# Kernel optimization log

Measured on AMD Instinct MI355X. Metric: run time of the kernel, lower is better.

The kernel has to match this reference:

```python
import jax, jax.numpy as jnp
import numpy as np

BATCH_SIZE = 512
N_PARTS = 4
TEMP_FAC = 0.1
D = 4096
EPS = 1e-6


def _static_indices():
    # bs and factor per the n_parts==4, batch_size!=12 branch
    bs = 4 * BATCH_SIZE
    factor = 10 * N_PARTS
    pos = np.arange(bs)
    active = pos[pos % (3 * N_PARTS) < N_PARTS]            # positions that contribute
    # i1..i6 = (pos + k*n_parts) % bs for k = 0..5
    I = (active[:, None] + np.arange(6)[None, :] * N_PARTS) % bs   # (P, 6)
    # denominator indices removed: (pos + k*n_parts) % bs for k = 0..factor*n_parts-1
    offs = (active[:, None] + np.arange(factor * N_PARTS)[None, :] * N_PARTS) % bs
    M = np.ones((active.shape[0], bs), dtype=np.float32)
    M[np.arange(active.shape[0])[:, None], offs] = 0.0     # (P, bs) denominator mask
    return I, M

_I, _M = _static_indices()
# symmetrical-loss pairs: (i1,i2),(i2,i3),(i1,i4),(i4,i5),(i5,i6),(i2,i5),(i3,i6)
_PAIRS = [(0, 1), (1, 2), (0, 3), (3, 4), (4, 5), (1, 4), (2, 5)]


def setup_inputs() -> dict:
    key = jax.random.key(0)
    reg_pred = jax.random.normal(key, (4 * BATCH_SIZE, D), dtype=jnp.float32)
    return {"reg_pred": reg_pred}


def reference(reg_pred):
    I = jnp.asarray(_I)
    M = jnp.asarray(_M)
    norms = jnp.linalg.norm(reg_pred, axis=1)              # (bs,)
    # torch CosineSimilarity: dot / max(||a||*||b||, eps)
    gram = reg_pred @ reg_pred.T                           # (bs, bs)
    S = gram / jnp.maximum(norms[:, None] * norms[None, :], EPS) / TEMP_FAC
    E = jnp.exp(S)                                         # (bs, bs)
    # denominator exp-sums for each anchor role k at each active position p
    Dsum = jnp.einsum('pkb,pb->pk', E[I], M)               # (P, 6)
    total = jnp.float32(0.0)
    for a, b in _PAIRS:
        num = S[I[:, a], I[:, b]]                          # (P,)
        en = jnp.exp(num)
        total = total + jnp.sum(-jnp.log(en / (en + Dsum[:, a]))
                                - jnp.log(en / (en + Dsum[:, b])))
    return total / (6 * BATCH_SIZE)
```

## Files before the change

### kernel.cpp

```cpp
#include <hip/hip_runtime.h>
#include <hip/hip_bf16.h>
#include <stdint.h>

#define NROWS 2048
#define DIM   4096
#define NACT  684
#define INV_TEMP 10.0f
#define NTILE 136
#define KSPLIT 4
#define KSEG  1024
#define KITER 32
#define FP8_SCALE 16.0f
#define PART_SCALE (1.0f / 256.0f)

#define WAITCNT_VM0   0x0F70
#define WAITCNT_VM2   0x0F72
#define WAITCNT_VM4   0x0F74
#define WAITCNT_VM6   0x0F76

typedef __attribute__((ext_vector_type(4))) float floatx4;
typedef __attribute__((ext_vector_type(8))) short shortx8;
typedef __attribute__((ext_vector_type(8))) unsigned short ushortx8;

static __device__ __forceinline__ unsigned short f32_to_bf16(float f) {
  union { float f; unsigned int u; } v; v.f = f;
  unsigned int u = v.u;
  unsigned int r = u + 0x7fffu + ((u >> 16) & 1u);
  return (unsigned short)(r >> 16);
}
static __device__ __forceinline__ float bf16_to_f32(unsigned short u) {
  union { unsigned int u; float f; } v; v.u = ((unsigned int)u) << 16;
  return v.f;
}
static __device__ __forceinline__ unsigned short f32_to_f16(float f) {
  _Float16 h = (_Float16)f;
  union { _Float16 h; unsigned short u; } v; v.h = h;
  return v.u;
}
static __device__ __forceinline__ float f16_to_f32(unsigned short u) {
  union { unsigned short u; _Float16 h; } v; v.u = u;
  return (float)v.h;
}

__global__ __launch_bounds__(256) void k_normconv_fp8(const float* __restrict__ X,
                                                      unsigned char* __restrict__ Yq) {
  const int row = blockIdx.x;
  const float4* xr = (const float4*)(X + (size_t)row * DIM);
  float4 v[4];
  float s = 0.f;
#pragma unroll
  for (int t = 0; t < 4; t++) {
    float4 w = xr[threadIdx.x * 4 + t];
    v[t] = w;
    s += w.x * w.x + w.y * w.y + w.z * w.z + w.w * w.w;
  }
#pragma unroll
  for (int off = 32; off > 0; off >>= 1) s += __shfl_down(s, off, 64);
  __shared__ float wsum[4];
  if ((threadIdx.x & 63) == 0) wsum[threadIdx.x >> 6] = s;
  __syncthreads();
  const float total = wsum[0] + wsum[1] + wsum[2] + wsum[3];
  const float sc = FP8_SCALE / fmaxf(sqrtf(total), 1e-30f);
  uint4 o;
  unsigned int r0;
  r0 = __builtin_amdgcn_cvt_pk_fp8_f32(v[0].x * sc, v[0].y * sc, 0, false);
  o.x = __builtin_amdgcn_cvt_pk_fp8_f32(v[0].z * sc, v[0].w * sc, r0, true);
  r0 = __builtin_amdgcn_cvt_pk_fp8_f32(v[1].x * sc, v[1].y * sc, 0, false);
  o.y = __builtin_amdgcn_cvt_pk_fp8_f32(v[1].z * sc, v[1].w * sc, r0, true);
  r0 = __builtin_amdgcn_cvt_pk_fp8_f32(v[2].x * sc, v[2].y * sc, 0, false);
  o.z = __builtin_amdgcn_cvt_pk_fp8_f32(v[2].z * sc, v[2].w * sc, r0, true);
  r0 = __builtin_amdgcn_cvt_pk_fp8_f32(v[3].x * sc, v[3].y * sc, 0, false);
  o.w = __builtin_amdgcn_cvt_pk_fp8_f32(v[3].z * sc, v[3].w * sc, r0, true);
  ((uint4*)(Yq + (size_t)row * DIM))[threadIdx.x] = o;
}

__global__ __launch_bounds__(256) void k_gemm_sym(const unsigned char* __restrict__ Yq,
                                                  unsigned short* __restrict__ P) {
  __shared__ __attribute__((aligned(16))) unsigned char lds[4 * 8192];
  const int bid = blockIdx.x;
  const int kz = bid & 3;
  const int t  = bid >> 2;
  int ti = 0, rem = t;
  while (rem >= 16 - ti) { rem -= 16 - ti; ti++; }
  const int tj = ti + rem;
  const int row0 = ti * 128;
  const int col0 = tj * 128;
  const int kbase = kz * KSEG;

  const int tid  = threadIdx.x;
  const int lane = tid & 63;
  const int wave = tid >> 6;
  const int wr = wave >> 1;
  const int wc = wave & 1;

  floatx4 zero = {0.f, 0.f, 0.f, 0.f};
  floatx4 acc[4][4];
#pragma unroll
  for (int i = 0; i < 4; i++)
#pragma unroll
    for (int j = 0; j < 4; j++) acc[i][j] = zero;

  const unsigned char* gA = Yq + (size_t)(row0 + (tid >> 1)) * DIM + kbase + (tid & 1) * 16;
  const unsigned char* gB = Yq + (size_t)(col0 + (tid >> 1)) * DIM + kbase + (tid & 1) * 16;

  const int fr  = lane & 15;
  const int fc8 = (lane >> 4) * 8;

#define ISSUE(st, koff)                                                                \
  do {                                                                                 \
    __builtin_amdgcn_global_load_lds(                                                  \
        (const __attribute__((address_space(1))) void*)(gA + (koff)),                  \
        (__attribute__((address_space(3))) void*)(lds + (st) * 8192 + tid * 16),       \
        16, 0, 0);                                                                     \
    __builtin_amdgcn_global_load_lds(                                                  \
        (const __attribute__((address_space(1))) void*)(gB + (koff)),                  \
        (__attribute__((address_space(3))) void*)(lds + (st) * 8192 + 4096 + tid * 16),\
        16, 0, 0);                                                                     \
  } while (0)

#define COMPUTE(st)                                                                    \
  do {                                                                                 \
    const unsigned char* bA = lds + (st) * 8192;                                       \
    const unsigned char* bB = bA + 4096;                                               \
    long long af[4], bf[4];                                                            \
    _Pragma("unroll")                                                                  \
    for (int mi = 0; mi < 4; mi++)                                                     \
      af[mi] = *(const long long*)(bA + (wr * 64 + mi * 16 + fr) * 32 + fc8);          \
    _Pragma("unroll")                                                                  \
    for (int ni = 0; ni < 4; ni++)                                                     \
      bf[ni] = *(const long long*)(bB + (wc * 64 + ni * 16 + fr) * 32 + fc8);          \
    _Pragma("unroll")                                                                  \
    for (int mi = 0; mi < 4; mi++)                                                     \
      _Pragma("unroll")                                                                \
      for (int ni = 0; ni < 4; ni++)                                                   \
        acc[mi][ni] = __builtin_amdgcn_mfma_f32_16x16x32_fp8_fp8(af[mi], bf[ni],       \
                                                                 acc[mi][ni], 0, 0, 0);\
  } while (0)

  ISSUE(0, 0);
  ISSUE(1, 32);
  ISSUE(2, 64);
#pragma unroll 4
  for (int k = 0; k < KITER; k++) {
    const int cur = k & 3;
    if (k < KITER - 3) {
      ISSUE((k + 3) & 3, (k + 3) * 32);
      __builtin_amdgcn_s_waitcnt(WAITCNT_VM6);
    } else if (k == KITER - 3) {
      __builtin_amdgcn_s_waitcnt(WAITCNT_VM4);
    } else if (k == KITER - 2) {
      __builtin_amdgcn_s_waitcnt(WAITCNT_VM2);
    } else {
      __builtin_amdgcn_s_waitcnt(WAITCNT_VM0);
    }
    __builtin_amdgcn_sched_barrier(0);
    __builtin_amdgcn_s_barrier();
    COMPUTE(cur);
    if (k < KITER - 1) {
      __builtin_amdgcn_s_barrier();
      __builtin_amdgcn_sched_barrier(0);
    }
  }

#undef ISSUE
#undef COMPUTE

  unsigned short* dst = P + (size_t)(t * KSPLIT + kz) * 16384;
  const int cc  = lane & 15;
  const int cr4 = (lane >> 4) * 4;
#pragma unroll
  for (int mi = 0; mi < 4; mi++) {
    const int row = wr * 64 + mi * 16 + cr4;
#pragma unroll
    for (int ni = 0; ni < 4; ni++) {
      const int col = wc * 64 + ni * 16 + cc;
      unsigned int d0 = (unsigned int)f32_to_bf16(acc[mi][ni][0] * PART_SCALE) |
                        ((unsigned int)f32_to_bf16(acc[mi][ni][1] * PART_SCALE) << 16);
      unsigned int d1 = (unsigned int)f32_to_bf16(acc[mi][ni][2] * PART_SCALE) |
                        ((unsigned int)f32_to_bf16(acc[mi][ni][3] * PART_SCALE) << 16);
      uint2 v; v.x = d0; v.y = d1;
      *(uint2*)(dst + (size_t)col * 128 + row) = v;
    }
  }
}

__global__ __launch_bounds__(256) void k_combine(const unsigned short* __restrict__ P,
                                                 unsigned short* __restrict__ S,
                                                 float* __restrict__ T) {
  __shared__ float tileS[32][132];
  __shared__ float tileE[32][132];
  const int t = blockIdx.x;
  const int h = blockIdx.y;
  int ti = 0, rem = t;
  while (rem >= 16 - ti) { rem -= 16 - ti; ti++; }
  const int tj = ti + rem;
  const int gr = ti * 128, gc = tj * 128;
  const int c0 = h * 32;
  const int tid = threadIdx.x;
  const int cl = tid >> 3;
  const int q  = tid & 7;

  float acc[16];
#pragma unroll
  for (int j = 0; j < 16; j++) acc[j] = 0.f;
#pragma unroll
  for (int kz = 0; kz < KSPLIT; kz++) {
    const ushortx8* p = (const ushortx8*)(P + (size_t)(t * KSPLIT + kz) * 16384 +
                                          (size_t)(c0 + cl) * 128 + q * 16);
#pragma unroll
    for (int c = 0; c < 2; c++) {
      ushortx8 u = p[c];
#pragma unroll
      for (int e = 0; e < 8; e++) acc[c * 8 + e] += bf16_to_f32((unsigned short)u[e]);
    }
  }
  float cs = 0.f;
  unsigned short hv[16];
#pragma unroll
  for (int j = 0; j < 16; j++) {
    float v = acc[j] * INV_TEMP;
    float ev = __expf(v);
    hv[j] = f32_to_f16(v);
    tileS[cl][q * 16 + j] = v;
    tileE[cl][q * 16 + j] = ev;
    cs += ev;
  }
  {
    uint4* srow = (uint4*)(S + (size_t)(gc + c0 + cl) * NROWS + gr + q * 16);
#pragma unroll
    for (int u = 0; u < 2; u++) {
      uint4 w;
      w.x = (unsigned int)hv[u * 8 + 0] | ((unsigned int)hv[u * 8 + 1] << 16);
      w.y = (unsigned int)hv[u * 8 + 2] | ((unsigned int)hv[u * 8 + 3] << 16);
      w.z = (unsigned int)hv[u * 8 + 4] | ((unsigned int)hv[u * 8 + 5] << 16);
      w.w = (unsigned int)hv[u * 8 + 6] | ((unsigned int)hv[u * 8 + 7] << 16);
      srow[u] = w;
    }
  }
  cs += __shfl_xor(cs, 1, 64);
  cs += __shfl_xor(cs, 2, 64);
  cs += __shfl_xor(cs, 4, 64);
  if (q == 0) atomicAdd(&T[gc + c0 + cl], cs);

  if (ti != tj) {
    __syncthreads();
    const int r = tid >> 1;
    const int hh = tid & 1;
    float rs = 0.f;
    unsigned short hv2[16];
#pragma unroll
    for (int e = 0; e < 16; e++) {
      hv2[e] = f32_to_f16(tileS[hh * 16 + e][r]);
      rs += tileE[hh * 16 + e][r];
    }
    uint4* drow = (uint4*)(S + (size_t)(gr + r) * NROWS + gc + c0 + hh * 16);
#pragma unroll
    for (int u = 0; u < 2; u++) {
      uint4 w;
      w.x = (unsigned int)hv2[u * 8 + 0] | ((unsigned int)hv2[u * 8 + 1] << 16);
      w.y = (unsigned int)hv2[u * 8 + 2] | ((unsigned int)hv2[u * 8 + 3] << 16);
      w.z = (unsigned int)hv2[u * 8 + 4] | ((unsigned int)hv2[u * 8 + 5] << 16);
      w.w = (unsigned int)hv2[u * 8 + 6] | ((unsigned int)hv2[u * 8 + 7] << 16);
      drow[u] = w;
    }
    rs += __shfl_xor(rs, 1, 64);
    if (hh == 0) atomicAdd(&T[gr + r], rs);
  }
}

__global__ __launch_bounds__(64) void k_dsum_h(const unsigned short* __restrict__ S,
                                               const float* __restrict__ T,
                                               float* __restrict__ Ds) {
  const int p = blockIdx.x;
  const int k = blockIdx.y;
  const int a = 12 * (p >> 2) + (p & 3);
  const int lane = threadIdx.x;
  const int row = (a + 4 * k) & (NROWS - 1);
  const int m = a >> 2;
  const int c = a & 3;
  const uint2* sr = (const uint2*)(S + (size_t)row * NROWS);
  float s = 0.f;
  {
    uint2 v0 = sr[(m + lane) & 511];
    uint2 v1 = sr[(m + 64 + lane) & 511];
    unsigned short e0 = (c < 2) ? (unsigned short)(v0.x >> (16 * c))
                                : (unsigned short)(v0.y >> (16 * (c - 2)));
    unsigned short e1 = (c < 2) ? (unsigned short)(v1.x >> (16 * c))
                                : (unsigned short)(v1.y >> (16 * (c - 2)));
    s += __expf(f16_to_f32(e0)) + __expf(f16_to_f32(e1));
    if (lane < 32) {
      uint2 v2 = sr[(m + 128 + lane) & 511];
      unsigned short e2 = (c < 2) ? (unsigned short)(v2.x >> (16 * c))
                                  : (unsigned short)(v2.y >> (16 * (c - 2)));
      s += __expf(f16_to_f32(e2));
    }
  }
#pragma unroll
  for (int off = 32; off > 0; off >>= 1) s += __shfl_down(s, off, 64);
  if (lane == 0) Ds[p * 6 + k] = T[row] - s;
}

__global__ __launch_bounds__(256) void k_final_h(const unsigned short* __restrict__ S,
                                                 const float* __restrict__ Ds,
                                                 float* __restrict__ out) {
  const int pa[7] = {0, 1, 0, 3, 4, 1, 2};
  const int pb[7] = {1, 2, 3, 4, 5, 4, 5};
  const int idx = blockIdx.x * 256 + threadIdx.x;
  float s = 0.f;
  if (idx < NACT * 7) {
    const int p = idx / 7;
    const int q = idx - p * 7;
    const int a0 = 12 * (p >> 2) + (p & 3);
    const int ra = (a0 + 4 * pa[q]) & (NROWS - 1);
    const int rb = (a0 + 4 * pb[q]) & (NROWS - 1);
    const float num = f16_to_f32(S[(size_t)ra * NROWS + rb]);
    const float en = __expf(num);
    s = __logf(en + Ds[p * 6 + pa[q]]) + __logf(en + Ds[p * 6 + pb[q]]) - 2.f * num;
  }
#pragma unroll
  for (int off = 32; off > 0; off >>= 1) s += __shfl_down(s, off, 64);
  if ((threadIdx.x & 63) == 0) atomicAdd(out, s * (1.0f / (6.0f * 512.0f)));
}

__global__ __launch_bounds__(256) void k_normconv(const float* __restrict__ X,
                                                  unsigned short* __restrict__ Y) {
  const int row = blockIdx.x;
  const float4* xr = (const float4*)(X + (size_t)row * DIM);
  float4 v[4];
  float s = 0.f;
#pragma unroll
  for (int t = 0; t < 4; t++) {
    float4 w = xr[threadIdx.x + t * 256];
    v[t] = w;
    s += w.x * w.x + w.y * w.y + w.z * w.z + w.w * w.w;
  }
#pragma unroll
  for (int off = 32; off > 0; off >>= 1) s += __shfl_down(s, off, 64);
  __shared__ float wsum[4];
  if ((threadIdx.x & 63) == 0) wsum[threadIdx.x >> 6] = s;
  __syncthreads();
  const float total = wsum[0] + wsum[1] + wsum[2] + wsum[3];
  const float inv = 1.0f / fmaxf(sqrtf(total), 1e-30f);
  ushort4* yr = (ushort4*)(Y + (size_t)row * DIM);
#pragma unroll
  for (int t = 0; t < 4; t++) {
    float4 w = v[t];
    ushort4 o;
    o.x = f32_to_bf16(w.x * inv);
    o.y = f32_to_bf16(w.y * inv);
    o.z = f32_to_bf16(w.z * inv);
    o.w = f32_to_bf16(w.w * inv);
    yr[threadIdx.x + t * 256] = o;
  }
}

__global__ __launch_bounds__(256) void k_gemm(const unsigned short* __restrict__ Y,
                                              float* __restrict__ S) {
  __shared__ __attribute__((aligned(16))) unsigned short sA[128 * 32];
  __shared__ __attribute__((aligned(16))) unsigned short sB[128 * 32];
  const int tid  = threadIdx.x;
  const int lane = tid & 63;
  const int wave = tid >> 6;
  const int wr = wave >> 1;
  const int wc = wave & 1;
  const int row0 = blockIdx.y * 128;
  const int col0 = blockIdx.x * 128;

  floatx4 zero = {0.f, 0.f, 0.f, 0.f};
  floatx4 acc[4][4];
#pragma unroll
  for (int i = 0; i < 4; i++)
#pragma unroll
    for (int j = 0; j < 4; j++) acc[i][j] = zero;

  const int sr = tid >> 2;
  const int sc = (tid & 3) * 8;
  const unsigned short* gA0 = Y + (size_t)(row0 + sr) * DIM + sc;
  const unsigned short* gA1 = gA0 + (size_t)64 * DIM;
  const unsigned short* gB0 = Y + (size_t)(col0 + sr) * DIM + sc;
  const unsigned short* gB1 = gB0 + (size_t)64 * DIM;

  const int fr = lane & 15;
  const int fc = (lane >> 4) * 8;

  for (int k0 = 0; k0 < DIM; k0 += 32) {
    __builtin_amdgcn_global_load_lds(
        (const __attribute__((address_space(1))) void*)(gA0 + k0),
        (__attribute__((address_space(3))) void*)(sA + tid * 8), 16, 0, 0);
    __builtin_amdgcn_global_load_lds(
        (const __attribute__((address_space(1))) void*)(gA1 + k0),
        (__attribute__((address_space(3))) void*)(sA + 2048 + tid * 8), 16, 0, 0);
    __builtin_amdgcn_global_load_lds(
        (const __attribute__((address_space(1))) void*)(gB0 + k0),
        (__attribute__((address_space(3))) void*)(sB + tid * 8), 16, 0, 0);
    __builtin_amdgcn_global_load_lds(
        (const __attribute__((address_space(1))) void*)(gB1 + k0),
        (__attribute__((address_space(3))) void*)(sB + 2048 + tid * 8), 16, 0, 0);
    __syncthreads();

    shortx8 af[4], bf[4];
#pragma unroll
    for (int mi = 0; mi < 4; mi++)
      af[mi] = *(const shortx8*)(sA + (wr * 64 + mi * 16 + fr) * 32 + fc);
#pragma unroll
    for (int ni = 0; ni < 4; ni++)
      bf[ni] = *(const shortx8*)(sB + (wc * 64 + ni * 16 + fr) * 32 + fc);
#pragma unroll
    for (int mi = 0; mi < 4; mi++)
#pragma unroll
      for (int ni = 0; ni < 4; ni++)
        acc[mi][ni] = __builtin_amdgcn_mfma_f32_16x16x32_bf16(af[mi], bf[ni], acc[mi][ni], 0, 0, 0);
    __syncthreads();
  }

  const int cc  = lane & 15;
  const int cr4 = (lane >> 4) * 4;
#pragma unroll
  for (int mi = 0; mi < 4; mi++) {
    const int row = row0 + wr * 64 + mi * 16 + cr4;
#pragma unroll
    for (int ni = 0; ni < 4; ni++) {
      const int col = col0 + wc * 64 + ni * 16 + cc;
      float* dst = S + (size_t)row * NROWS + col;
#pragma unroll
      for (int r = 0; r < 4; r++) dst[(size_t)r * NROWS] = acc[mi][ni][r] * INV_TEMP;
    }
  }
}

__global__ __launch_bounds__(256) void k_rowsum(const float* __restrict__ S,
                                                float* __restrict__ T) {
  const int row = blockIdx.x;
  const float* sr = S + (size_t)row * NROWS;
  float s = 0.f;
  for (int b = threadIdx.x; b < NROWS; b += 256) s += __expf(sr[b]);
#pragma unroll
  for (int off = 32; off > 0; off >>= 1) s += __shfl_down(s, off, 64);
  __shared__ float wsum[4];
  if ((threadIdx.x & 63) == 0) wsum[threadIdx.x >> 6] = s;
  __syncthreads();
  if (threadIdx.x == 0) T[row] = wsum[0] + wsum[1] + wsum[2] + wsum[3];
}

__global__ __launch_bounds__(64) void k_dsum(const float* __restrict__ S,
                                             const float* __restrict__ T,
                                             float* __restrict__ Ds) {
  const int p = blockIdx.x;
  const int k = blockIdx.y;
  const int a = 12 * (p >> 2) + (p & 3);
  const int lane = threadIdx.x;
  const int row = (a + 4 * k) & (NROWS - 1);
  const int m = a >> 2;
  const int c = a & 3;
  const float4* sr4 = (const float4*)(S + (size_t)row * NROWS);
  float s = 0.f;
  {
    float4 v0 = sr4[(m + lane) & 511];
    float4 v1 = sr4[(m + 64 + lane) & 511];
    float e0 = c == 0 ? v0.x : c == 1 ? v0.y : c == 2 ? v0.z : v0.w;
    float e1 = c == 0 ? v1.x : c == 1 ? v1.y : c == 2 ? v1.z : v1.w;
    s += __expf(e0) + __expf(e1);
    if (lane < 32) {
      float4 v2 = sr4[(m + 128 + lane) & 511];
      float e2 = c == 0 ? v2.x : c == 1 ? v2.y : c == 2 ? v2.z : v2.w;
      s += __expf(e2);
    }
  }
#pragma unroll
  for (int off = 32; off > 0; off >>= 1) s += __shfl_down(s, off, 64);
  if (lane == 0) Ds[p * 6 + k] = T[row] - s;
}

__global__ __launch_bounds__(256) void k_final(const float* __restrict__ S,
                                               const float* __restrict__ Ds,
                                               float* __restrict__ out) {
  const int pa[7] = {0, 1, 0, 3, 4, 1, 2};
  const int pb[7] = {1, 2, 3, 4, 5, 4, 5};
  const int idx = blockIdx.x * 256 + threadIdx.x;
  float s = 0.f;
  if (idx < NACT * 7) {
    const int p = idx / 7;
    const int q = idx - p * 7;
    const int a0 = 12 * (p >> 2) + (p & 3);
    const int ra = (a0 + 4 * pa[q]) & (NROWS - 1);
    const int rb = (a0 + 4 * pb[q]) & (NROWS - 1);
    const float num = S[(size_t)ra * NROWS + rb];
    const float en = __expf(num);
    s = __logf(en + Ds[p * 6 + pa[q]]) + __logf(en + Ds[p * 6 + pb[q]]) - 2.f * num;
  }
#pragma unroll
  for (int off = 32; off > 0; off >>= 1) s += __shfl_down(s, off, 64);
  if ((threadIdx.x & 63) == 0) atomicAdd(out, s * (1.0f / (6.0f * 512.0f)));
}

extern "C" void kernel_launch(void* const* d_in, const int* in_sizes, int n_in,
                              void* d_out, int out_size, void* d_ws, size_t ws_size,
                              hipStream_t stream) {
  const float* X = (const float*)d_in[0];
  char* ws = (char*)d_ws;
  float* out = (float*)d_out;

  const size_t pOff = (size_t)32 * 1024 * 1024;
  const size_t pBytes = (size_t)NTILE * KSPLIT * 16384 * 2;
  const size_t needA = pOff + pBytes + 8192 + NACT * 6 * 4 + 256;

  hipMemsetAsync(out, 0, sizeof(float), stream);

  if (ws_size >= needA) {
    unsigned char* Yq = (unsigned char*)ws;
    unsigned short* S16 = (unsigned short*)(ws + (size_t)16 * 1024 * 1024);
    unsigned short* P = (unsigned short*)(ws + pOff);
    float* T  = (float*)(ws + pOff + pBytes);
    float* Ds = (float*)(ws + pOff + pBytes + 8192);
    hipMemsetAsync(T, 0, NROWS * sizeof(float), stream);
    hipLaunchKernelGGL(k_normconv_fp8, dim3(NROWS), dim3(256), 0, stream, X, Yq);
    hipLaunchKernelGGL(k_gemm_sym, dim3(NTILE * KSPLIT), dim3(256), 0, stream, Yq, P);
    hipLaunchKernelGGL(k_combine, dim3(NTILE, 4), dim3(256), 0, stream, P, S16, T);
    hipLaunchKernelGGL(k_dsum_h, dim3(NACT, 6), dim3(64), 0, stream, S16, T, Ds);
    hipLaunchKernelGGL(k_final_h, dim3((NACT * 7 + 255) / 256), dim3(256), 0, stream, S16, Ds, out);
  } else {
    unsigned short* Y = (unsigned short*)ws;
    float* S = (float*)(ws + (size_t)16 * 1024 * 1024);
    float* T  = (float*)(ws + pOff);
    float* Ds = (float*)(ws + pOff + 8192);
    hipLaunchKernelGGL(k_normconv, dim3(NROWS), dim3(256), 0, stream, X, Y);
    hipLaunchKernelGGL(k_gemm, dim3(16, 16), dim3(256), 0, stream, Y, S);
    hipLaunchKernelGGL(k_rowsum, dim3(NROWS), dim3(256), 0, stream, S, T);
    hipLaunchKernelGGL(k_dsum, dim3(NACT, 6), dim3(64), 0, stream, S, T, Ds);
    hipLaunchKernelGGL(k_final, dim3((NACT * 7 + 255) / 256), dim3(256), 0, stream, S, Ds, out);
  }
}
```

Baseline: 121.4 us.

## Use 256x256 symmetric GEMM tiles with 8-way K split and fuse tail kernels

```diff
diff --git a/kernel.cpp b/kernel.cpp
--- a/kernel.cpp
+++ b/kernel.cpp
@@ -6,17 +6,16 @@
 #define DIM   4096
 #define NACT  684
 #define INV_TEMP 10.0f
-#define NTILE 136
-#define KSPLIT 4
-#define KSEG  1024
-#define KITER 32
+#define NT256 36
+#define KSPLIT 8
+#define KSEG  512
+#define KITER 16
 #define FP8_SCALE 16.0f
 #define PART_SCALE (1.0f / 256.0f)
 
 #define WAITCNT_VM0   0x0F70
 #define WAITCNT_VM2   0x0F72
 #define WAITCNT_VM4   0x0F74
-#define WAITCNT_VM6   0x0F76
 
 typedef __attribute__((ext_vector_type(4))) float floatx4;
 typedef __attribute__((ext_vector_type(8))) short shortx8;
@@ -74,17 +73,17 @@
   ((uint4*)(Yq + (size_t)row * DIM))[threadIdx.x] = o;
 }
 
-__global__ __launch_bounds__(256) void k_gemm_sym(const unsigned char* __restrict__ Yq,
-                                                  unsigned short* __restrict__ P) {
-  __shared__ __attribute__((aligned(16))) unsigned char lds[4 * 8192];
+__global__ __launch_bounds__(512, 2) void k_gemm_sym(const unsigned char* __restrict__ Yq,
+                                                     unsigned short* __restrict__ P) {
+  __shared__ __attribute__((aligned(16))) unsigned char lds[3 * 16384];
   const int bid = blockIdx.x;
-  const int kz = bid & 3;
-  const int t  = bid >> 2;
+  const int kz = bid & 7;
+  const int t  = bid >> 3;
   int ti = 0, rem = t;
-  while (rem >= 16 - ti) { rem -= 16 - ti; ti++; }
+  while (rem >= 8 - ti) { rem -= 8 - ti; ti++; }
   const int tj = ti + rem;
-  const int row0 = ti * 128;
-  const int col0 = tj * 128;
+  const int row0 = ti * 256;
+  const int col0 = tj * 256;
   const int kbase = kz * KSEG;
 
   const int tid  = threadIdx.x;
@@ -94,11 +93,11 @@
   const int wc = wave & 1;
 
   floatx4 zero = {0.f, 0.f, 0.f, 0.f};
-  floatx4 acc[4][4];
+  floatx4 acc[4][8];
 #pragma unroll
   for (int i = 0; i < 4; i++)
 #pragma unroll
-    for (int j = 0; j < 4; j++) acc[i][j] = zero;
+    for (int j = 0; j < 8; j++) acc[i][j] = zero;
 
   const unsigned char* gA = Yq + (size_t)(row0 + (tid >> 1)) * DIM + kbase + (tid & 1) * 16;
   const unsigned char* gB = Yq + (size_t)(col0 + (tid >> 1)) * DIM + kbase + (tid & 1) * 16;
@@ -106,47 +105,44 @@
   const int fr  = lane & 15;
   const int fc8 = (lane >> 4) * 8;
 
-#define ISSUE(st, koff)                                                                \
-  do {                                                                                 \
-    __builtin_amdgcn_global_load_lds(                                                  \
-        (const __attribute__((address_space(1))) void*)(gA + (koff)),                  \
-        (__attribute__((address_space(3))) void*)(lds + (st) * 8192 + tid * 16),       \
-        16, 0, 0);                                                                     \
-    __builtin_amdgcn_global_load_lds(                                                  \
-        (const __attribute__((address_space(1))) void*)(gB + (koff)),                  \
-        (__attribute__((address_space(3))) void*)(lds + (st) * 8192 + 4096 + tid * 16),\
-        16, 0, 0);                                                                     \
+#define ISSUE(st, koff)                                                                 \
+  do {                                                                                  \
+    __builtin_amdgcn_global_load_lds(                                                   \
+        (const __attribute__((address_space(1))) void*)(gA + (koff)),                   \
+        (__attribute__((address_space(3))) void*)(lds + (st) * 16384 + tid * 16),       \
+        16, 0, 0);                                                                      \
+    __builtin_amdgcn_global_load_lds(                                                   \
+        (const __attribute__((address_space(1))) void*)(gB + (koff)),                   \
+        (__attribute__((address_space(3))) void*)(lds + (st) * 16384 + 8192 + tid * 16),\
+        16, 0, 0);                                                                      \
   } while (0)
 
-#define COMPUTE(st)                                                                    \
-  do {                                                                                 \
-    const unsigned char* bA = lds + (st) * 8192;                                       \
-    const unsigned char* bB = bA + 4096;                                               \
-    long long af[4], bf[4];                                                            \
-    _Pragma("unroll")                                                                  \
-    for (int mi = 0; mi < 4; mi++)                                                     \
-      af[mi] = *(const long long*)(bA + (wr * 64 + mi * 16 + fr) * 32 + fc8);          \
-    _Pragma("unroll")                                                                  \
-    for (int ni = 0; ni < 4; ni++)                                                     \
-      bf[ni] = *(const long long*)(bB + (wc * 64 + ni * 16 + fr) * 32 + fc8);          \
-    _Pragma("unroll")                                                                  \
-    for (int mi = 0; mi < 4; mi++)                                                     \
-      _Pragma("unroll")                                                                \
-      for (int ni = 0; ni < 4; ni++)                                                   \
-        acc[mi][ni] = __builtin_amdgcn_mfma_f32_16x16x32_fp8_fp8(af[mi], bf[ni],       \
-                                                                 acc[mi][ni], 0, 0, 0);\
+#define COMPUTE(st)                                                                     \
+  do {                                                                                  \
+    const unsigned char* bA = lds + (st) * 16384;                                       \
+    const unsigned char* bB = bA + 8192;                                                \
+    long long af[4], bf[8];                                                             \
+    _Pragma("unroll")                                                                   \
+    for (int mi = 0; mi < 4; mi++)                                                      \
+      af[mi] = *(const long long*)(bA + (wr * 64 + mi * 16 + fr) * 32 + fc8);           \
+    _Pragma("unroll")                                                                   \
+    for (int ni = 0; ni < 8; ni++)                                                      \
+      bf[ni] = *(const long long*)(bB + (wc * 128 + ni * 16 + fr) * 32 + fc8);          \
+    _Pragma("unroll")                                                                   \
+    for (int mi = 0; mi < 4; mi++)                                                      \
+      _Pragma("unroll")                                                                 \
+      for (int ni = 0; ni < 8; ni++)                                                    \
+        acc[mi][ni] = __builtin_amdgcn_mfma_f32_16x16x32_fp8_fp8(af[mi], bf[ni],        \
+                                                                 acc[mi][ni], 0, 0, 0); \
   } while (0)
 
   ISSUE(0, 0);
   ISSUE(1, 32);
-  ISSUE(2, 64);
-#pragma unroll 4
+#pragma unroll
   for (int k = 0; k < KITER; k++) {
-    const int cur = k & 3;
-    if (k < KITER - 3) {
-      ISSUE((k + 3) & 3, (k + 3) * 32);
-      __builtin_amdgcn_s_waitcnt(WAITCNT_VM6);
-    } else if (k == KITER - 3) {
+    const int cur = k % 3;
+    if (k < KITER - 2) {
+      ISSUE((k + 2) % 3, (k + 2) * 32);
       __builtin_amdgcn_s_waitcnt(WAITCNT_VM4);
     } else if (k == KITER - 2) {
       __builtin_amdgcn_s_waitcnt(WAITCNT_VM2);
@@ -165,21 +161,21 @@
 #undef ISSUE
 #undef COMPUTE
 
-  unsigned short* dst = P + (size_t)(t * KSPLIT + kz) * 16384;
+  unsigned short* dst = P + (size_t)(t * KSPLIT + kz) * 65536;
   const int cc  = lane & 15;
   const int cr4 = (lane >> 4) * 4;
 #pragma unroll
   for (int mi = 0; mi < 4; mi++) {
     const int row = wr * 64 + mi * 16 + cr4;
 #pragma unroll
-    for (int ni = 0; ni < 4; ni++) {
-      const int col = wc * 64 + ni * 16 + cc;
+    for (int ni = 0; ni < 8; ni++) {
+      const int col = wc * 128 + ni * 16 + cc;
       unsigned int d0 = (unsigned int)f32_to_bf16(acc[mi][ni][0] * PART_SCALE) |
                         ((unsigned int)f32_to_bf16(acc[mi][ni][1] * PART_SCALE) << 16);
       unsigned int d1 = (unsigned int)f32_to_bf16(acc[mi][ni][2] * PART_SCALE) |
                         ((unsigned int)f32_to_bf16(acc[mi][ni][3] * PART_SCALE) << 16);
       uint2 v; v.x = d0; v.y = d1;
-      *(uint2*)(dst + (size_t)col * 128 + row) = v;
+      *(uint2*)(dst + (size_t)col * 256 + row) = v;
     }
   }
 }
@@ -187,26 +183,26 @@
 __global__ __launch_bounds__(256) void k_combine(const unsigned short* __restrict__ P,
                                                  unsigned short* __restrict__ S,
                                                  float* __restrict__ T) {
-  __shared__ float tileS[32][132];
-  __shared__ float tileE[32][132];
+  __shared__ float tileS[16][258];
+  __shared__ float tileE[16][258];
   const int t = blockIdx.x;
   const int h = blockIdx.y;
   int ti = 0, rem = t;
-  while (rem >= 16 - ti) { rem -= 16 - ti; ti++; }
+  while (rem >= 8 - ti) { rem -= 8 - ti; ti++; }
   const int tj = ti + rem;
-  const int gr = ti * 128, gc = tj * 128;
-  const int c0 = h * 32;
+  const int gr = ti * 256, gc = tj * 256;
+  const int c0 = h * 16;
   const int tid = threadIdx.x;
-  const int cl = tid >> 3;
-  const int q  = tid & 7;
+  const int cl = tid >> 4;
+  const int q  = tid & 15;
 
   float acc[16];
 #pragma unroll
   for (int j = 0; j < 16; j++) acc[j] = 0.f;
 #pragma unroll
   for (int kz = 0; kz < KSPLIT; kz++) {
-    const ushortx8* p = (const ushortx8*)(P + (size_t)(t * KSPLIT + kz) * 16384 +
-                                          (size_t)(c0 + cl) * 128 + q * 16);
+    const ushortx8* p = (const ushortx8*)(P + (size_t)(t * KSPLIT + kz) * 65536 +
+                                          (size_t)(c0 + cl) * 256 + q * 16);
 #pragma unroll
     for (int c = 0; c < 2; c++) {
       ushortx8 u = p[c];
@@ -240,20 +236,20 @@
   cs += __shfl_xor(cs, 1, 64);
   cs += __shfl_xor(cs, 2, 64);
   cs += __shfl_xor(cs, 4, 64);
+  cs += __shfl_xor(cs, 8, 64);
   if (q == 0) atomicAdd(&T[gc + c0 + cl], cs);
 
   if (ti != tj) {
     __syncthreads();
-    const int r = tid >> 1;
-    const int hh = tid & 1;
+    const int r = tid;
     float rs = 0.f;
     unsigned short hv2[16];
 #pragma unroll
-    for (int e = 0; e < 16; e++) {
-      hv2[e] = f32_to_f16(tileS[hh * 16 + e][r]);
-      rs += tileE[hh * 16 + e][r];
-    }
-    uint4* drow = (uint4*)(S + (size_t)(gr + r) * NROWS + gc + c0 + hh * 16);
+    for (int c = 0; c < 16; c++) {
+      hv2[c] = f32_to_f16(tileS[c][r]);
+      rs += tileE[c][r];
+    }
+    uint4* drow = (uint4*)(S + (size_t)(gr + r) * NROWS + gc + c0);
 #pragma unroll
     for (int u = 0; u < 2; u++) {
       uint4 w;
@@ -263,24 +259,24 @@
       w.w = (unsigned int)hv2[u * 8 + 6] | ((unsigned int)hv2[u * 8 + 7] << 16);
       drow[u] = w;
     }
-    rs += __shfl_xor(rs, 1, 64);
-    if (hh == 0) atomicAdd(&T[gr + r], rs);
-  }
-}
-
-__global__ __launch_bounds__(64) void k_dsum_h(const unsigned short* __restrict__ S,
-                                               const float* __restrict__ T,
-                                               float* __restrict__ Ds) {
+    atomicAdd(&T[gr + r], rs);
+  }
+}
+
+__global__ __launch_bounds__(64) void k_tail(const unsigned short* __restrict__ S,
+                                             const float* __restrict__ T,
+                                             float* __restrict__ out) {
   const int p = blockIdx.x;
-  const int k = blockIdx.y;
   const int a = 12 * (p >> 2) + (p & 3);
   const int lane = threadIdx.x;
-  const int row = (a + 4 * k) & (NROWS - 1);
   const int m = a >> 2;
   const int c = a & 3;
-  const uint2* sr = (const uint2*)(S + (size_t)row * NROWS);
-  float s = 0.f;
-  {
+  __shared__ float Dsh[6];
+#pragma unroll
+  for (int k = 0; k < 6; k++) {
+    const int row = (a + 4 * k) & (NROWS - 1);
+    const uint2* sr = (const uint2*)(S + (size_t)row * NROWS);
+    float s = 0.f;
     uint2 v0 = sr[(m + lane) & 511];
     uint2 v1 = sr[(m + 64 + lane) & 511];
     unsigned short e0 = (c < 2) ? (unsigned short)(v0.x >> (16 * c))
@@ -294,32 +290,24 @@
                                   : (unsigned short)(v2.y >> (16 * (c - 2)));
       s += __expf(f16_to_f32(e2));
     }
-  }
-#pragma unroll
-  for (int off = 32; off > 0; off >>= 1) s += __shfl_down(s, off, 64);
-  if (lane == 0) Ds[p * 6 + k] = T[row] - s;
-}
-
-__global__ __launch_bounds__(256) void k_final_h(const unsigned short* __restrict__ S,
-                                                 const float* __restrict__ Ds,
-                                                 float* __restrict__ out) {
+#pragma unroll
+    for (int off = 32; off > 0; off >>= 1) s += __shfl_down(s, off, 64);
+    if (lane == 0) Dsh[k] = T[row] - s;
+  }
+  __syncthreads();
   const int pa[7] = {0, 1, 0, 3, 4, 1, 2};
   const int pb[7] = {1, 2, 3, 4, 5, 4, 5};
-  const int idx = blockIdx.x * 256 + threadIdx.x;
-  float s = 0.f;
-  if (idx < NACT * 7) {
-    const int p = idx / 7;
-    const int q = idx - p * 7;
-    const int a0 = 12 * (p >> 2) + (p & 3);
-    const int ra = (a0 + 4 * pa[q]) & (NROWS - 1);
-    const int rb = (a0 + 4 * pb[q]) & (NROWS - 1);
+  float s2 = 0.f;
+  if (lane < 7) {
+    const int ra = (a + 4 * pa[lane]) & (NROWS - 1);
+    const int rb = (a + 4 * pb[lane]) & (NROWS - 1);
     const float num = f16_to_f32(S[(size_t)ra * NROWS + rb]);
     const float en = __expf(num);
-    s = __logf(en + Ds[p * 6 + pa[q]]) + __logf(en + Ds[p * 6 + pb[q]]) - 2.f * num;
-  }
-#pragma unroll
-  for (int off = 32; off > 0; off >>= 1) s += __shfl_down(s, off, 64);
-  if ((threadIdx.x & 63) == 0) atomicAdd(out, s * (1.0f / (6.0f * 512.0f)));
+    s2 = __logf(en + Dsh[pa[lane]]) + __logf(en + Dsh[pb[lane]]) - 2.f * num;
+  }
+#pragma unroll
+  for (int off = 32; off > 0; off >>= 1) s2 += __shfl_down(s2, off, 64);
+  if (lane == 0) atomicAdd(out, s2 * (1.0f / (6.0f * 512.0f)));
 }
 
 __global__ __launch_bounds__(256) void k_normconv(const float* __restrict__ X,
@@ -500,29 +488,29 @@
   char* ws = (char*)d_ws;
   float* out = (float*)d_out;
 
-  const size_t pOff = (size_t)32 * 1024 * 1024;
-  const size_t pBytes = (size_t)NTILE * KSPLIT * 16384 * 2;
-  const size_t needA = pOff + pBytes + 8192 + NACT * 6 * 4 + 256;
+  const size_t pOffA  = (size_t)8 * 1024 * 1024;
+  const size_t pBytesA = (size_t)NT256 * KSPLIT * 65536 * 2;
+  const size_t sOffA  = (size_t)46 * 1024 * 1024;
+  const size_t tOffA  = (size_t)54 * 1024 * 1024;
+  const size_t needA  = tOffA + NROWS * 4 + 256;
 
   hipMemsetAsync(out, 0, sizeof(float), stream);
 
   if (ws_size >= needA) {
     unsigned char* Yq = (unsigned char*)ws;
-    unsigned short* S16 = (unsigned short*)(ws + (size_t)16 * 1024 * 1024);
-    unsigned short* P = (unsigned short*)(ws + pOff);
-    float* T  = (float*)(ws + pOff + pBytes);
-    float* Ds = (float*)(ws + pOff + pBytes + 8192);
+    unsigned short* P = (unsigned short*)(ws + pOffA);
+    unsigned short* S16 = (unsigned short*)(ws + sOffA);
+    float* T = (float*)(ws + tOffA);
     hipMemsetAsync(T, 0, NROWS * sizeof(float), stream);
     hipLaunchKernelGGL(k_normconv_fp8, dim3(NROWS), dim3(256), 0, stream, X, Yq);
-    hipLaunchKernelGGL(k_gemm_sym, dim3(NTILE * KSPLIT), dim3(256), 0, stream, Yq, P);
-    hipLaunchKernelGGL(k_combine, dim3(NTILE, 4), dim3(256), 0, stream, P, S16, T);
-    hipLaunchKernelGGL(k_dsum_h, dim3(NACT, 6), dim3(64), 0, stream, S16, T, Ds);
-    hipLaunchKernelGGL(k_final_h, dim3((NACT * 7 + 255) / 256), dim3(256), 0, stream, S16, Ds, out);
+    hipLaunchKernelGGL(k_gemm_sym, dim3(NT256 * KSPLIT), dim3(512), 0, stream, Yq, P);
+    hipLaunchKernelGGL(k_combine, dim3(NT256, 16), dim3(256), 0, stream, P, S16, T);
+    hipLaunchKernelGGL(k_tail, dim3(NACT), dim3(64), 0, stream, S16, T, out);
   } else {
     unsigned short* Y = (unsigned short*)ws;
     float* S = (float*)(ws + (size_t)16 * 1024 * 1024);
-    float* T  = (float*)(ws + pOff);
-    float* Ds = (float*)(ws + pOff + 8192);
+    float* T  = (float*)(ws + (size_t)32 * 1024 * 1024);
+    float* Ds = (float*)(ws + (size_t)32 * 1024 * 1024 + 8192);
     hipLaunchKernelGGL(k_normconv, dim3(NROWS), dim3(256), 0, stream, X, Y);
     hipLaunchKernelGGL(k_gemm, dim3(16, 16), dim3(256), 0, stream, Y, S);
     hipLaunchKernelGGL(k_rowsum, dim3(NROWS), dim3(256), 0, stream, S, T);
```

After: 155.4 us. 1.28x slower.

## Double K-step per pipeline stage in fp8 GEMM and fuse dsum with final loss

Applied to the files above, without the earlier changes.

```diff
diff --git a/kernel.cpp b/kernel.cpp
--- a/kernel.cpp
+++ b/kernel.cpp
@@ -9,14 +9,13 @@
 #define NTILE 136
 #define KSPLIT 4
 #define KSEG  1024
-#define KITER 32
+#define KITER 16
 #define FP8_SCALE 16.0f
 #define PART_SCALE (1.0f / 256.0f)
 
 #define WAITCNT_VM0   0x0F70
-#define WAITCNT_VM2   0x0F72
 #define WAITCNT_VM4   0x0F74
-#define WAITCNT_VM6   0x0F76
+#define WAITCNT_VM8   0x0F78
 
 typedef __attribute__((ext_vector_type(4))) float floatx4;
 typedef __attribute__((ext_vector_type(8))) short shortx8;
@@ -76,7 +75,7 @@
 
 __global__ __launch_bounds__(256) void k_gemm_sym(const unsigned char* __restrict__ Yq,
                                                   unsigned short* __restrict__ P) {
-  __shared__ __attribute__((aligned(16))) unsigned char lds[4 * 8192];
+  __shared__ __attribute__((aligned(16))) unsigned char lds[3 * 16384];
   const int bid = blockIdx.x;
   const int kz = bid & 3;
   const int t  = bid >> 2;
@@ -106,50 +105,56 @@
   const int fr  = lane & 15;
   const int fc8 = (lane >> 4) * 8;
 
-#define ISSUE(st, koff)                                                                \
-  do {                                                                                 \
-    __builtin_amdgcn_global_load_lds(                                                  \
-        (const __attribute__((address_space(1))) void*)(gA + (koff)),                  \
-        (__attribute__((address_space(3))) void*)(lds + (st) * 8192 + tid * 16),       \
-        16, 0, 0);                                                                     \
-    __builtin_amdgcn_global_load_lds(                                                  \
-        (const __attribute__((address_space(1))) void*)(gB + (koff)),                  \
-        (__attribute__((address_space(3))) void*)(lds + (st) * 8192 + 4096 + tid * 16),\
-        16, 0, 0);                                                                     \
+#define ISSUE(st, koff)                                                                  \
+  do {                                                                                   \
+    unsigned char* base = lds + (st) * 16384;                                            \
+    __builtin_amdgcn_global_load_lds(                                                    \
+        (const __attribute__((address_space(1))) void*)(gA + (koff)),                    \
+        (__attribute__((address_space(3))) void*)(base + tid * 16), 16, 0, 0);           \
+    __builtin_amdgcn_global_load_lds(                                                    \
+        (const __attribute__((address_space(1))) void*)(gA + (koff) + 32),               \
+        (__attribute__((address_space(3))) void*)(base + 4096 + tid * 16), 16, 0, 0);    \
+    __builtin_amdgcn_global_load_lds(                                                    \
+        (const __attribute__((address_space(1))) void*)(gB + (koff)),                    \
+        (__attribute__((address_space(3))) void*)(base + 8192 + tid * 16), 16, 0, 0);    \
+    __builtin_amdgcn_global_load_lds(                                                    \
+        (const __attribute__((address_space(1))) void*)(gB + (koff) + 32),               \
+        (__attribute__((address_space(3))) void*)(base + 12288 + tid * 16), 16, 0, 0);   \
   } while (0)
 
-#define COMPUTE(st)                                                                    \
-  do {                                                                                 \
-    const unsigned char* bA = lds + (st) * 8192;                                       \
-    const unsigned char* bB = bA + 4096;                                               \
-    long long af[4], bf[4];                                                            \
-    _Pragma("unroll")                                                                  \
-    for (int mi = 0; mi < 4; mi++)                                                     \
-      af[mi] = *(const long long*)(bA + (wr * 64 + mi * 16 + fr) * 32 + fc8);          \
-    _Pragma("unroll")                                                                  \
-    for (int ni = 0; ni < 4; ni++)                                                     \
-      bf[ni] = *(const long long*)(bB + (wc * 64 + ni * 16 + fr) * 32 + fc8);          \
-    _Pragma("unroll")                                                                  \
-    for (int mi = 0; mi < 4; mi++)                                                     \
-      _Pragma("unroll")                                                                \
-      for (int ni = 0; ni < 4; ni++)                                                   \
-        acc[mi][ni] = __builtin_amdgcn_mfma_f32_16x16x32_fp8_fp8(af[mi], bf[ni],       \
-                                                                 acc[mi][ni], 0, 0, 0);\
+#define COMPUTE(st)                                                                      \
+  do {                                                                                   \
+    const unsigned char* base = lds + (st) * 16384;                                      \
+    _Pragma("unroll")                                                                    \
+    for (int h = 0; h < 2; h++) {                                                        \
+      const unsigned char* bA = base + h * 4096;                                         \
+      const unsigned char* bB = base + 8192 + h * 4096;                                  \
+      long long af[4], bf[4];                                                            \
+      _Pragma("unroll")                                                                  \
+      for (int mi = 0; mi < 4; mi++)                                                     \
+        af[mi] = *(const long long*)(bA + (wr * 64 + mi * 16 + fr) * 32 + fc8);          \
+      _Pragma("unroll")                                                                  \
+      for (int ni = 0; ni < 4; ni++)                                                     \
+        bf[ni] = *(const long long*)(bB + (wc * 64 + ni * 16 + fr) * 32 + fc8);          \
+      _Pragma("unroll")                                                                  \
+      for (int mi = 0; mi < 4; mi++)                                                     \
+        _Pragma("unroll")                                                                \
+        for (int ni = 0; ni < 4; ni++)                                                   \
+          acc[mi][ni] = __builtin_amdgcn_mfma_f32_16x16x32_fp8_fp8(af[mi], bf[ni],       \
+                                                                   acc[mi][ni], 0, 0, 0);\
+    }                                                                                    \
   } while (0)
 
   ISSUE(0, 0);
-  ISSUE(1, 32);
-  ISSUE(2, 64);
+  ISSUE(1, 64);
 #pragma unroll 4
   for (int k = 0; k < KITER; k++) {
-    const int cur = k & 3;
-    if (k < KITER - 3) {
-      ISSUE((k + 3) & 3, (k + 3) * 32);
-      __builtin_amdgcn_s_waitcnt(WAITCNT_VM6);
-    } else if (k == KITER - 3) {
+    const int cur = k % 3;
+    if (k < KITER - 2) {
+      ISSUE((k + 2) % 3, (k + 2) * 64);
+      __builtin_amdgcn_s_waitcnt(WAITCNT_VM8);
+    } else if (k == KITER - 2) {
       __builtin_amdgcn_s_waitcnt(WAITCNT_VM4);
-    } else if (k == KITER - 2) {
-      __builtin_amdgcn_s_waitcnt(WAITCNT_VM2);
     } else {
       __builtin_amdgcn_s_waitcnt(WAITCNT_VM0);
     }
@@ -268,19 +273,20 @@
   }
 }
 
-__global__ __launch_bounds__(64) void k_dsum_h(const unsigned short* __restrict__ S,
-                                               const float* __restrict__ T,
-                                               float* __restrict__ Ds) {
+__global__ __launch_bounds__(64) void k_tail(const unsigned short* __restrict__ S,
+                                             const float* __restrict__ T,
+                                             float* __restrict__ out) {
   const int p = blockIdx.x;
-  const int k = blockIdx.y;
   const int a = 12 * (p >> 2) + (p & 3);
   const int lane = threadIdx.x;
-  const int row = (a + 4 * k) & (NROWS - 1);
   const int m = a >> 2;
   const int c = a & 3;
-  const uint2* sr = (const uint2*)(S + (size_t)row * NROWS);
-  float s = 0.f;
-  {
+  __shared__ float Dsh[6];
+#pragma unroll
+  for (int k = 0; k < 6; k++) {
+    const int row = (a + 4 * k) & (NROWS - 1);
+    const uint2* sr = (const uint2*)(S + (size_t)row * NROWS);
+    float s = 0.f;
     uint2 v0 = sr[(m + lane) & 511];
     uint2 v1 = sr[(m + 64 + lane) & 511];
     unsigned short e0 = (c < 2) ? (unsigned short)(v0.x >> (16 * c))
@@ -294,32 +300,24 @@
                                   : (unsigned short)(v2.y >> (16 * (c - 2)));
       s += __expf(f16_to_f32(e2));
     }
-  }
-#pragma unroll
-  for (int off = 32; off > 0; off >>= 1) s += __shfl_down(s, off, 64);
-  if (lane == 0) Ds[p * 6 + k] = T[row] - s;
-}
-
-__global__ __launch_bounds__(256) void k_final_h(const unsigned short* __restrict__ S,
-                                                 const float* __restrict__ Ds,
-                                                 float* __restrict__ out) {
+#pragma unroll
+    for (int off = 32; off > 0; off >>= 1) s += __shfl_down(s, off, 64);
+    if (lane == 0) Dsh[k] = T[row] - s;
+  }
+  __syncthreads();
   const int pa[7] = {0, 1, 0, 3, 4, 1, 2};
   const int pb[7] = {1, 2, 3, 4, 5, 4, 5};
-  const int idx = blockIdx.x * 256 + threadIdx.x;
-  float s = 0.f;
-  if (idx < NACT * 7) {
-    const int p = idx / 7;
-    const int q = idx - p * 7;
-    const int a0 = 12 * (p >> 2) + (p & 3);
-    const int ra = (a0 + 4 * pa[q]) & (NROWS - 1);
-    const int rb = (a0 + 4 * pb[q]) & (NROWS - 1);
+  float s2 = 0.f;
+  if (lane < 7) {
+    const int ra = (a + 4 * pa[lane]) & (NROWS - 1);
+    const int rb = (a + 4 * pb[lane]) & (NROWS - 1);
     const float num = f16_to_f32(S[(size_t)ra * NROWS + rb]);
     const float en = __expf(num);
-    s = __logf(en + Ds[p * 6 + pa[q]]) + __logf(en + Ds[p * 6 + pb[q]]) - 2.f * num;
-  }
-#pragma unroll
-  for (int off = 32; off > 0; off >>= 1) s += __shfl_down(s, off, 64);
-  if ((threadIdx.x & 63) == 0) atomicAdd(out, s * (1.0f / (6.0f * 512.0f)));
+    s2 = __logf(en + Dsh[pa[lane]]) + __logf(en + Dsh[pb[lane]]) - 2.f * num;
+  }
+#pragma unroll
+  for (int off = 32; off > 0; off >>= 1) s2 += __shfl_down(s2, off, 64);
+  if (lane == 0) atomicAdd(out, s2 * (1.0f / (6.0f * 512.0f)));
 }
 
 __global__ __launch_bounds__(256) void k_normconv(const float* __restrict__ X,
@@ -502,7 +500,7 @@
 
   const size_t pOff = (size_t)32 * 1024 * 1024;
   const size_t pBytes = (size_t)NTILE * KSPLIT * 16384 * 2;
-  const size_t needA = pOff + pBytes + 8192 + NACT * 6 * 4 + 256;
+  const size_t needA = pOff + pBytes + 8192 + 256;
 
   hipMemsetAsync(out, 0, sizeof(float), stream);
 
@@ -510,14 +508,12 @@
     unsigned char* Yq = (unsigned char*)ws;
     unsigned short* S16 = (unsigned short*)(ws + (size_t)16 * 1024 * 1024);
     unsigned short* P = (unsigned short*)(ws + pOff);
-    float* T  = (float*)(ws + pOff + pBytes);
-    float* Ds = (float*)(ws + pOff + pBytes + 8192);
+    float* T = (float*)(ws + pOff + pBytes);
     hipMemsetAsync(T, 0, NROWS * sizeof(float), stream);
     hipLaunchKernelGGL(k_normconv_fp8, dim3(NROWS), dim3(256), 0, stream, X, Yq);
     hipLaunchKernelGGL(k_gemm_sym, dim3(NTILE * KSPLIT), dim3(256), 0, stream, Yq, P);
     hipLaunchKernelGGL(k_combine, dim3(NTILE, 4), dim3(256), 0, stream, P, S16, T);
-    hipLaunchKernelGGL(k_dsum_h, dim3(NACT, 6), dim3(64), 0, stream, S16, T, Ds);
-    hipLaunchKernelGGL(k_final_h, dim3((NACT * 7 + 255) / 256), dim3(256), 0, stream, S16, Ds, out);
+    hipLaunchKernelGGL(k_tail, dim3(NACT), dim3(64), 0, stream, S16, T, out);
   } else {
     unsigned short* Y = (unsigned short*)ws;
     float* S = (float*)(ws + (size_t)16 * 1024 * 1024);
```

New measurement: 128.6 us. 5.9% more time.

## Give each wave private LDS buffers and drop block barriers in fp8 GEMM

Applied to the files above, without the earlier changes.

```diff
diff --git a/kernel.cpp b/kernel.cpp
--- a/kernel.cpp
+++ b/kernel.cpp
@@ -14,9 +14,8 @@
 #define PART_SCALE (1.0f / 256.0f)
 
 #define WAITCNT_VM0   0x0F70
-#define WAITCNT_VM2   0x0F72
 #define WAITCNT_VM4   0x0F74
-#define WAITCNT_VM6   0x0F76
+#define WAITCNT_VM8   0x0F78
 
 typedef __attribute__((ext_vector_type(4))) float floatx4;
 typedef __attribute__((ext_vector_type(8))) short shortx8;
@@ -76,15 +75,13 @@
 
 __global__ __launch_bounds__(256) void k_gemm_sym(const unsigned char* __restrict__ Yq,
                                                   unsigned short* __restrict__ P) {
-  __shared__ __attribute__((aligned(16))) unsigned char lds[4 * 8192];
+  __shared__ __attribute__((aligned(16))) unsigned char lds[4 * 12288];
   const int bid = blockIdx.x;
   const int kz = bid & 3;
   const int t  = bid >> 2;
   int ti = 0, rem = t;
   while (rem >= 16 - ti) { rem -= 16 - ti; ti++; }
   const int tj = ti + rem;
-  const int row0 = ti * 128;
-  const int col0 = tj * 128;
   const int kbase = kz * KSEG;
 
   const int tid  = threadIdx.x;
@@ -92,6 +89,10 @@
   const int wave = tid >> 6;
   const int wr = wave >> 1;
   const int wc = wave & 1;
+  const int row0 = ti * 128 + wr * 64;
+  const int col0 = tj * 128 + wc * 64;
+
+  unsigned char* wbase = lds + wave * 12288;
 
   floatx4 zero = {0.f, 0.f, 0.f, 0.f};
   floatx4 acc[4][4];
@@ -100,66 +101,64 @@
 #pragma unroll
     for (int j = 0; j < 4; j++) acc[i][j] = zero;
 
-  const unsigned char* gA = Yq + (size_t)(row0 + (tid >> 1)) * DIM + kbase + (tid & 1) * 16;
-  const unsigned char* gB = Yq + (size_t)(col0 + (tid >> 1)) * DIM + kbase + (tid & 1) * 16;
+  const unsigned char* gA = Yq + (size_t)(row0 + (lane >> 1)) * DIM + kbase + (lane & 1) * 16;
+  const unsigned char* gB = Yq + (size_t)(col0 + (lane >> 1)) * DIM + kbase + (lane & 1) * 16;
 
   const int fr  = lane & 15;
   const int fc8 = (lane >> 4) * 8;
 
-#define ISSUE(st, koff)                                                                \
-  do {                                                                                 \
-    __builtin_amdgcn_global_load_lds(                                                  \
-        (const __attribute__((address_space(1))) void*)(gA + (koff)),                  \
-        (__attribute__((address_space(3))) void*)(lds + (st) * 8192 + tid * 16),       \
-        16, 0, 0);                                                                     \
-    __builtin_amdgcn_global_load_lds(                                                  \
-        (const __attribute__((address_space(1))) void*)(gB + (koff)),                  \
-        (__attribute__((address_space(3))) void*)(lds + (st) * 8192 + 4096 + tid * 16),\
-        16, 0, 0);                                                                     \
+#define ISSUE(st, koff)                                                                  \
+  do {                                                                                   \
+    unsigned char* sA = wbase + (st) * 4096;                                             \
+    unsigned char* sB = sA + 2048;                                                       \
+    __builtin_amdgcn_global_load_lds(                                                    \
+        (const __attribute__((address_space(1))) void*)(gA + (koff)),                    \
+        (__attribute__((address_space(3))) void*)(sA + lane * 16), 16, 0, 0);            \
+    __builtin_amdgcn_global_load_lds(                                                    \
+        (const __attribute__((address_space(1))) void*)(gA + (size_t)32 * DIM + (koff)), \
+        (__attribute__((address_space(3))) void*)(sA + 1024 + lane * 16), 16, 0, 0);     \
+    __builtin_amdgcn_global_load_lds(                                                    \
+        (const __attribute__((address_space(1))) void*)(gB + (koff)),                    \
+        (__attribute__((address_space(3))) void*)(sB + lane * 16), 16, 0, 0);            \
+    __builtin_amdgcn_global_load_lds(                                                    \
+        (const __attribute__((address_space(1))) void*)(gB + (size_t)32 * DIM + (koff)), \
+        (__attribute__((address_space(3))) void*)(sB + 1024 + lane * 16), 16, 0, 0);     \
   } while (0)
 
-#define COMPUTE(st)                                                                    \
-  do {                                                                                 \
-    const unsigned char* bA = lds + (st) * 8192;                                       \
-    const unsigned char* bB = bA + 4096;                                               \
-    long long af[4], bf[4];                                                            \
-    _Pragma("unroll")                                                                  \
-    for (int mi = 0; mi < 4; mi++)                                                     \
-      af[mi] = *(const long long*)(bA + (wr * 64 + mi * 16 + fr) * 32 + fc8);          \
-    _Pragma("unroll")                                                                  \
-    for (int ni = 0; ni < 4; ni++)                                                     \
-      bf[ni] = *(const long long*)(bB + (wc * 64 + ni * 16 + fr) * 32 + fc8);          \
-    _Pragma("unroll")                                                                  \
-    for (int mi = 0; mi < 4; mi++)                                                     \
-      _Pragma("unroll")                                                                \
-      for (int ni = 0; ni < 4; ni++)                                                   \
-        acc[mi][ni] = __builtin_amdgcn_mfma_f32_16x16x32_fp8_fp8(af[mi], bf[ni],       \
-                                                                 acc[mi][ni], 0, 0, 0);\
+#define COMPUTE(st)                                                                      \
+  do {                                                                                   \
+    const unsigned char* bA = wbase + (st) * 4096;                                       \
+    const unsigned char* bB = bA + 2048;                                                 \
+    long long af[4], bf[4];                                                              \
+    _Pragma("unroll")                                                                    \
+    for (int mi = 0; mi < 4; mi++)                                                       \
+      af[mi] = *(const long long*)(bA + (mi * 16 + fr) * 32 + fc8);                      \
+    _Pragma("unroll")                                                                    \
+    for (int ni = 0; ni < 4; ni++)                                                       \
+      bf[ni] = *(const long long*)(bB + (ni * 16 + fr) * 32 + fc8);                      \
+    _Pragma("unroll")                                                                    \
+    for (int mi = 0; mi < 4; mi++)                                                       \
+      _Pragma("unroll")                                                                  \
+      for (int ni = 0; ni < 4; ni++)                                                     \
+        acc[mi][ni] = __builtin_amdgcn_mfma_f32_16x16x32_fp8_fp8(af[mi], bf[ni],         \
+                                                                 acc[mi][ni], 0, 0, 0);  \
   } while (0)
 
   ISSUE(0, 0);
   ISSUE(1, 32);
-  ISSUE(2, 64);
-#pragma unroll 4
+#pragma unroll
   for (int k = 0; k < KITER; k++) {
-    const int cur = k & 3;
-    if (k < KITER - 3) {
-      ISSUE((k + 3) & 3, (k + 3) * 32);
-      __builtin_amdgcn_s_waitcnt(WAITCNT_VM6);
-    } else if (k == KITER - 3) {
+    const int cur = k % 3;
+    if (k < KITER - 2) {
+      ISSUE((k + 2) % 3, (k + 2) * 32);
+      __builtin_amdgcn_s_waitcnt(WAITCNT_VM8);
+    } else if (k == KITER - 2) {
       __builtin_amdgcn_s_waitcnt(WAITCNT_VM4);
-    } else if (k == KITER - 2) {
-      __builtin_amdgcn_s_waitcnt(WAITCNT_VM2);
     } else {
       __builtin_amdgcn_s_waitcnt(WAITCNT_VM0);
     }
     __builtin_amdgcn_sched_barrier(0);
-    __builtin_amdgcn_s_barrier();
     COMPUTE(cur);
-    if (k < KITER - 1) {
-      __builtin_amdgcn_s_barrier();
-      __builtin_amdgcn_sched_barrier(0);
-    }
   }
 
 #undef ISSUE
```

Result: no change. 123.1 us (+1.3%).
